# Kernel optimization log

Measured on AMD Instinct MI355X. Metric: run time of the kernel, lower is better.

Reference implementation:

```python
import jax, jax.numpy as jnp
import numpy as np

B, D = 4, 4            # batch, days
N = 5000               # node_number
V = 256                # congestion_space_dimension
F = 64                 # in_channels
C = 32                 # out_channels per head
H = 4                  # heads
E = 80000              # edges per graph (before self loops)
NEG_SLOPE = 0.2        # PyG GATConv default negative_slope


def setup_inputs() -> dict:
    key = jax.random.key(0)
    ks = jax.random.split(key, 7)
    x = jax.random.randint(ks[0], (B, D, N), 0, V)
    adjacency = jax.random.randint(ks[1], (2, E), 0, N)
    emb = jax.random.normal(ks[2], (V, F), dtype=jnp.float32)
    W = jax.random.normal(ks[3], (F, H * C), dtype=jnp.float32) * 0.1
    att_src = jax.random.normal(ks[4], (H, C), dtype=jnp.float32) * 0.1
    att_dst = jax.random.normal(ks[5], (H, C), dtype=jnp.float32) * 0.1
    bias = jnp.zeros((H * C,), dtype=jnp.float32)
    return {"x": x, "adjacency": adjacency, "emb": emb, "W": W,
            "att_src": att_src, "att_dst": att_dst, "bias": bias}


def reference(x, adjacency, emb, W, att_src, att_dst, bias):
    G = B * D
    feats = emb[x].reshape(G, N, F)                       # [G,N,F] embedding lookup
    # PyG GATConv adds self loops by default
    loops = jnp.arange(N)
    src = jnp.concatenate([adjacency[0], loops])          # [Et]
    dst = jnp.concatenate([adjacency[1], loops])          # [Et]
    xw = jnp.einsum('gnf,fk->gnk', feats, W).reshape(G, N, H, C)
    a_s = jnp.einsum('gnhc,hc->gnh', xw, att_src)         # [G,N,H]
    a_d = jnp.einsum('gnhc,hc->gnh', xw, att_dst)
    e = jax.nn.leaky_relu(a_s[:, src] + a_d[:, dst], NEG_SLOPE)  # [G,Et,H]
    # per-destination segment softmax (stable)
    seg_max = jax.vmap(lambda v: jax.ops.segment_max(v, dst, num_segments=N))(e)
    alpha = jnp.exp(e - seg_max[:, dst])
    denom = jax.vmap(lambda v: jax.ops.segment_sum(v, dst, num_segments=N))(alpha)
    alpha = alpha / denom[:, dst]                         # [G,Et,H]
    msg = alpha[..., None] * xw[:, src]                   # [G,Et,H,C]
    out = jax.vmap(lambda m: jax.ops.segment_sum(m, dst, num_segments=N))(msg)
    out = out.reshape(G, N, H * C) + bias                 # concat heads + bias
    return out.reshape(B, D, N * H * C)
```

## Files before the change

kernel.cpp:

```cpp
#include <hip/hip_runtime.h>
#include <math.h>

#define NN 5000
#define GG 16
#define VV 256
#define FF 64
#define HH 4
#define CC 32
#define HC 128
#define EE 80000
#define NEG 0.2f
#define WPB 4
#define SLOT 48
#define SPAD 50

__global__ void k_tables(const float* __restrict__ emb, const float* __restrict__ W,
                         const float* __restrict__ att_src, const float* __restrict__ att_dst,
                         float* __restrict__ T, float* __restrict__ as_t, float* __restrict__ ad_t,
                         int* __restrict__ cnt) {
  if (blockIdx.x >= VV) {
    int n = (blockIdx.x - VV) * 128 + threadIdx.x;
    if (n < NN) cnt[n] = 1;
    return;
  }
  __shared__ float se[FF];
  __shared__ float sT[HC];
  const int v = blockIdx.x;
  const int k = threadIdx.x;
  if (k < FF) se[k] = emb[v * FF + k];
  __syncthreads();
  float acc = 0.f;
#pragma unroll
  for (int f = 0; f < FF; ++f) acc += se[f] * W[f * HC + k];
  T[v * HC + k] = acc;
  sT[k] = acc;
  __syncthreads();
  if (k < 2 * HH) {
    const int h = k >> 1;
    const float* att = (k & 1) ? att_dst : att_src;
    float s = 0.f;
#pragma unroll
    for (int c = 0; c < CC; ++c) s += sT[h * CC + c] * att[h * CC + c];
    if (k & 1) ad_t[v * HH + h] = s;
    else       as_t[v * HH + h] = s;
  }
}

__global__ void k_count(const int* __restrict__ dst, int* __restrict__ cnt) {
  int e = blockIdx.x * blockDim.x + threadIdx.x;
  if (e < EE) atomicAdd(&cnt[dst[e]], 1);
}

__global__ void k_scan(const int* __restrict__ cnt, int* __restrict__ off,
                       int* __restrict__ cursor, int* __restrict__ csr) {
  __shared__ int part[256];
  const int t = threadIdx.x;
  const int CH = (NN + 255) / 256;
  const int i0 = t * CH;
  int lc[CH];
  int lsum = 0;
#pragma unroll
  for (int j = 0; j < CH; ++j) {
    int idx = i0 + j;
    int c = (idx < NN) ? cnt[idx] : 0;
    lc[j] = c;
    lsum += c;
  }
  part[t] = lsum;
  __syncthreads();
  for (int d = 1; d < 256; d <<= 1) {
    int val = (t >= d) ? part[t - d] : 0;
    __syncthreads();
    part[t] += val;
    __syncthreads();
  }
  int run = (t > 0) ? part[t - 1] : 0;
#pragma unroll
  for (int j = 0; j < CH; ++j) {
    int idx = i0 + j;
    if (idx < NN) {
      off[idx] = run;
      cursor[idx] = run + 1;
      csr[run] = idx;
      run += lc[j];
    }
  }
  if (t == 255) off[NN] = part[255];
}

#define NSCAT ((EE + 255) / 256)
__global__ void k_scatter_p(const int* __restrict__ src, const int* __restrict__ dst,
                            int* __restrict__ cursor, int* __restrict__ csr,
                            const float* __restrict__ as_t, const float* __restrict__ ad_t,
                            float* __restrict__ P) {
  if (blockIdx.x < NSCAT) {
    int e = blockIdx.x * 256 + threadIdx.x;
    if (e < EE) {
      int d = dst[e];
      int pos = atomicAdd(&cursor[d], 1);
      csr[pos] = src[e];
    }
    return;
  }
  const int d = blockIdx.x - NSCAT;
  const int v = threadIdx.x;
  const float4 a = ((const float4*)as_t)[v];
  const float4 b = ((const float4*)ad_t)[d];
  float e0 = a.x + b.x; e0 = e0 > 0.f ? e0 : NEG * e0;
  float e1 = a.y + b.y; e1 = e1 > 0.f ? e1 : NEG * e1;
  float e2 = a.z + b.z; e2 = e2 > 0.f ? e2 : NEG * e2;
  float e3 = a.w + b.w; e3 = e3 > 0.f ? e3 : NEG * e3;
  float4 p;
  p.x = __expf(e0); p.y = __expf(e1); p.z = __expf(e2); p.w = __expf(e3);
  ((float4*)P)[d * VV + v] = p;
}

__global__ __launch_bounds__(256)
void k_gat(const int* __restrict__ x, const int* __restrict__ off,
           const int* __restrict__ csr, const float* __restrict__ T,
           const float* __restrict__ P, const float* __restrict__ bias,
           float* __restrict__ out) {
  __shared__ float4 s_p4[WPB][4][SPAD];
  __shared__ int    s_ofs[WPB][4][SPAD];

  const int tid  = threadIdx.x;
  const int wave = tid >> 6;
  const int lane = tid & 63;
  const int sub  = lane >> 4;
  const int sl   = lane & 15;
  const int head = sl >> 2;

  const int w    = blockIdx.x * WPB + wave;
  const int inst = w * 4 + sub;
  const int g    = inst / NN;
  const int n    = inst - g * NN;

  const int base = off[n];
  const int deg  = off[n + 1] - base;
  const int xd   = x[inst];
  const float4* __restrict__ Pd = ((const float4*)P) + xd * VV;
  const int* __restrict__ xg = x + g * NN;

  const int my_ch = sl * 8;
  const float4 b0 = ((const float4*)bias)[sl * 2];
  const float4 b1 = ((const float4*)bias)[sl * 2 + 1];

  float4 dsum = make_float4(0.f, 0.f, 0.f, 0.f);
  float4 a0 = make_float4(0.f, 0.f, 0.f, 0.f);
  float4 a1 = make_float4(0.f, 0.f, 0.f, 0.f);

  for (int c0 = 0; c0 < deg; c0 += SLOT) {
    const int len = min(SLOT, deg - c0);
    for (int r = sl; r < len; r += 16) {
      const int srcn = csr[base + c0 + r];
      const int xv   = xg[srcn];
      const float4 p4 = Pd[xv];
      dsum.x += p4.x; dsum.y += p4.y; dsum.z += p4.z; dsum.w += p4.w;
      s_p4[wave][sub][r]  = p4;
      s_ofs[wave][sub][r] = xv << 7;
    }
    __threadfence_block();
#pragma unroll 2
    for (int j = 0; j < len; ++j) {
      const int   ofs = s_ofs[wave][sub][j];
      const float p   = ((const float*)&s_p4[wave][sub][j])[head];
      const float4 t0 = *(const float4*)&T[ofs + my_ch];
      const float4 t1 = *(const float4*)&T[ofs + my_ch + 4];
      a0.x += p * t0.x; a0.y += p * t0.y; a0.z += p * t0.z; a0.w += p * t0.w;
      a1.x += p * t1.x; a1.y += p * t1.y; a1.z += p * t1.z; a1.w += p * t1.w;
    }
    __threadfence_block();
  }

#pragma unroll
  for (int d = 1; d < 16; d <<= 1) {
    dsum.x += __shfl_xor(dsum.x, d);
    dsum.y += __shfl_xor(dsum.y, d);
    dsum.z += __shfl_xor(dsum.z, d);
    dsum.w += __shfl_xor(dsum.w, d);
  }
  const float den = (head == 0) ? dsum.x : (head == 1) ? dsum.y
                   : (head == 2) ? dsum.z : dsum.w;
  const float r = 1.f / den;

  float4 o0, o1;
  o0.x = a0.x * r + b0.x; o0.y = a0.y * r + b0.y;
  o0.z = a0.z * r + b0.z; o0.w = a0.w * r + b0.w;
  o1.x = a1.x * r + b1.x; o1.y = a1.y * r + b1.y;
  o1.z = a1.z * r + b1.z; o1.w = a1.w * r + b1.w;
  float* op = out + (size_t)inst * HC + my_ch;
  *(float4*)op = o0;
  *(float4*)(op + 4) = o1;
}

extern "C" void kernel_launch(void* const* d_in, const int* in_sizes, int n_in,
                              void* d_out, int out_size, void* d_ws, size_t ws_size,
                              hipStream_t stream) {
  const int*   x       = (const int*)d_in[0];
  const int*   adj     = (const int*)d_in[1];
  const float* emb     = (const float*)d_in[2];
  const float* W       = (const float*)d_in[3];
  const float* att_src = (const float*)d_in[4];
  const float* att_dst = (const float*)d_in[5];
  const float* bias    = (const float*)d_in[6];
  float*       out     = (float*)d_out;

  const int* adj_src = adj;
  const int* adj_dst = adj + EE;

  char* wp = (char*)d_ws;
  float* T    = (float*)wp; wp += (size_t)VV * HC * 4;
  float* as_t = (float*)wp; wp += (size_t)VV * HH * 4;
  float* ad_t = (float*)wp; wp += (size_t)VV * HH * 4;
  int* cnt    = (int*)wp;   wp += (size_t)NN * 4;
  int* off    = (int*)wp;   wp += (size_t)(NN + 4) * 4;
  int* cursor = (int*)wp;   wp += (size_t)NN * 4;
  int* csr    = (int*)wp;   wp += (size_t)(EE + NN) * 4;
  float* P    = (float*)wp; wp += (size_t)VV * VV * HH * 4;

  const int initblk = (NN + 127) / 128;
  k_tables<<<VV + initblk, 128, 0, stream>>>(emb, W, att_src, att_dst, T, as_t, ad_t, cnt);
  k_count<<<(EE + 255) / 256, 256, 0, stream>>>(adj_dst, cnt);
  k_scan<<<1, 256, 0, stream>>>(cnt, off, cursor, csr);
  k_scatter_p<<<NSCAT + VV, 256, 0, stream>>>(adj_src, adj_dst, cursor, csr, as_t, ad_t, P);
  k_gat<<<(GG * NN / 4) / WPB, 256, 0, stream>>>(x, off, csr, T, P, bias, out);
}
```

Before: 139.2 us.

## Fuse preprocessing into cooperative kernel and pre-gather source embedding ids per graph

Merges the four preprocessing launches into one cooperative kernel with grid-wide syncs, and falls back to separate launches if the cooperative launch fails. The CSR scatter now writes, for each of the 16 graphs, the source node's embedding index directly (csr_x). This removes the dependent csr→x double indirection in the main GAT loop and replaces it with one contiguous load. In exchange the scatter writes a 16x larger array (about 5.4 MB), and grid.sync adds its own overhead.

```diff
diff --git a/kernel.cpp b/kernel.cpp
--- a/kernel.cpp
+++ b/kernel.cpp
@@ -1,5 +1,8 @@
 #include <hip/hip_runtime.h>
+#include <hip/hip_cooperative_groups.h>
 #include <math.h>
+
+namespace cg = cooperative_groups;
 
 #define NN 5000
 #define GG 16
@@ -9,55 +12,73 @@
 #define CC 32
 #define HC 128
 #define EE 80000
+#define ET (EE + NN)
 #define NEG 0.2f
 #define WPB 4
 #define SLOT 48
 #define SPAD 50
-
-__global__ void k_tables(const float* __restrict__ emb, const float* __restrict__ W,
-                         const float* __restrict__ att_src, const float* __restrict__ att_dst,
-                         float* __restrict__ T, float* __restrict__ as_t, float* __restrict__ ad_t,
-                         int* __restrict__ cnt) {
-  if (blockIdx.x >= VV) {
-    int n = (blockIdx.x - VV) * 128 + threadIdx.x;
-    if (n < NN) cnt[n] = 1;
-    return;
-  }
-  __shared__ float se[FF];
-  __shared__ float sT[HC];
-  const int v = blockIdx.x;
-  const int k = threadIdx.x;
-  if (k < FF) se[k] = emb[v * FF + k];
-  __syncthreads();
-  float acc = 0.f;
-#pragma unroll
-  for (int f = 0; f < FF; ++f) acc += se[f] * W[f * HC + k];
-  T[v * HC + k] = acc;
-  sT[k] = acc;
-  __syncthreads();
-  if (k < 2 * HH) {
-    const int h = k >> 1;
-    const float* att = (k & 1) ? att_dst : att_src;
-    float s = 0.f;
-#pragma unroll
-    for (int c = 0; c < CC; ++c) s += sT[h * CC + c] * att[h * CC + c];
-    if (k & 1) ad_t[v * HH + h] = s;
-    else       as_t[v * HH + h] = s;
-  }
-}
-
-__global__ void k_count(const int* __restrict__ dst, int* __restrict__ cnt) {
-  int e = blockIdx.x * blockDim.x + threadIdx.x;
-  if (e < EE) atomicAdd(&cnt[dst[e]], 1);
-}
-
-__global__ void k_scan(const int* __restrict__ cnt, int* __restrict__ off,
-                       int* __restrict__ cursor, int* __restrict__ csr) {
-  __shared__ int part[256];
-  const int t = threadIdx.x;
+#define NTASK (GG * NN / 4)
+#define PREP_BLOCKS 512
+
+union PrepS {
+  struct { float se[FF]; float sT[HC]; } tab;
+  int part[256];
+};
+
+__device__ __forceinline__ void phase0(PrepS& sm, int b, int t, int stride,
+                                       const float* __restrict__ emb, const float* __restrict__ W,
+                                       const float* __restrict__ att_src, const float* __restrict__ att_dst,
+                                       float* __restrict__ T, float* __restrict__ as_t,
+                                       float* __restrict__ ad_t, int* __restrict__ cnt) {
+  for (int i = b * 256 + t; i < NN; i += stride) cnt[i] = 0;
+  if (b < VV) {
+    const int v = b;
+    if (t < FF) sm.tab.se[t] = emb[v * FF + t];
+    __syncthreads();
+    if (t < HC) {
+      float acc = 0.f;
+#pragma unroll
+      for (int f = 0; f < FF; ++f) acc += sm.tab.se[f] * W[f * HC + t];
+      T[v * HC + t] = acc;
+      sm.tab.sT[t] = acc;
+    }
+    __syncthreads();
+    if (t < 2 * HH) {
+      const int h = t >> 1;
+      const float* att = (t & 1) ? att_dst : att_src;
+      float s = 0.f;
+#pragma unroll
+      for (int c = 0; c < CC; ++c) s += sm.tab.sT[h * CC + c] * att[h * CC + c];
+      if (t & 1) ad_t[v * HH + h] = s;
+      else       as_t[v * HH + h] = s;
+    }
+  }
+}
+
+__device__ __forceinline__ void phase1(int b, int t, int stride,
+                                       const int* __restrict__ adj_dst, int* __restrict__ cnt,
+                                       const float* __restrict__ as_t, const float* __restrict__ ad_t,
+                                       float* __restrict__ P) {
+  for (int e = b * 256 + t; e < EE; e += stride) atomicAdd(&cnt[adj_dst[e]], 1);
+  if (b >= VV && b < 2 * VV) {
+    const int d = b - VV;
+    const float4 a4 = ((const float4*)as_t)[t];
+    const float4 d4 = ((const float4*)ad_t)[d];
+    float e0 = a4.x + d4.x; e0 = e0 > 0.f ? e0 : NEG * e0;
+    float e1 = a4.y + d4.y; e1 = e1 > 0.f ? e1 : NEG * e1;
+    float e2 = a4.z + d4.z; e2 = e2 > 0.f ? e2 : NEG * e2;
+    float e3 = a4.w + d4.w; e3 = e3 > 0.f ? e3 : NEG * e3;
+    float4 p;
+    p.x = __expf(e0); p.y = __expf(e1); p.z = __expf(e2); p.w = __expf(e3);
+    ((float4*)P)[d * VV + t] = p;
+  }
+}
+
+__device__ __forceinline__ void phase2(PrepS& sm, int t, const int* __restrict__ cnt,
+                                       int* __restrict__ off, int* __restrict__ cursor) {
   const int CH = (NN + 255) / 256;
   const int i0 = t * CH;
-  int lc[CH];
+  int lc[(NN + 255) / 256];
   int lsum = 0;
 #pragma unroll
   for (int j = 0; j < CH; ++j) {
@@ -66,58 +87,93 @@
     lc[j] = c;
     lsum += c;
   }
-  part[t] = lsum;
+  sm.part[t] = lsum;
   __syncthreads();
   for (int d = 1; d < 256; d <<= 1) {
-    int val = (t >= d) ? part[t - d] : 0;
-    __syncthreads();
-    part[t] += val;
-    __syncthreads();
-  }
-  int run = (t > 0) ? part[t - 1] : 0;
+    int val = (t >= d) ? sm.part[t - d] : 0;
+    __syncthreads();
+    sm.part[t] += val;
+    __syncthreads();
+  }
+  int run = (t > 0) ? sm.part[t - 1] : 0;
 #pragma unroll
   for (int j = 0; j < CH; ++j) {
     int idx = i0 + j;
     if (idx < NN) {
-      off[idx] = run;
-      cursor[idx] = run + 1;
-      csr[run] = idx;
+      int o = run + idx;
+      off[idx] = o;
+      cursor[idx] = o + 1;
       run += lc[j];
     }
   }
-  if (t == 255) off[NN] = part[255];
-}
-
-#define NSCAT ((EE + 255) / 256)
-__global__ void k_scatter_p(const int* __restrict__ src, const int* __restrict__ dst,
-                            int* __restrict__ cursor, int* __restrict__ csr,
-                            const float* __restrict__ as_t, const float* __restrict__ ad_t,
-                            float* __restrict__ P) {
-  if (blockIdx.x < NSCAT) {
-    int e = blockIdx.x * 256 + threadIdx.x;
-    if (e < EE) {
-      int d = dst[e];
-      int pos = atomicAdd(&cursor[d], 1);
-      csr[pos] = src[e];
-    }
-    return;
-  }
-  const int d = blockIdx.x - NSCAT;
-  const int v = threadIdx.x;
-  const float4 a = ((const float4*)as_t)[v];
-  const float4 b = ((const float4*)ad_t)[d];
-  float e0 = a.x + b.x; e0 = e0 > 0.f ? e0 : NEG * e0;
-  float e1 = a.y + b.y; e1 = e1 > 0.f ? e1 : NEG * e1;
-  float e2 = a.z + b.z; e2 = e2 > 0.f ? e2 : NEG * e2;
-  float e3 = a.w + b.w; e3 = e3 > 0.f ? e3 : NEG * e3;
-  float4 p;
-  p.x = __expf(e0); p.y = __expf(e1); p.z = __expf(e2); p.w = __expf(e3);
-  ((float4*)P)[d * VV + v] = p;
+  if (t == 255) off[NN] = sm.part[255] + NN;
+}
+
+__device__ __forceinline__ void phase3(int b, int t, int stride,
+                                       const int* __restrict__ x,
+                                       const int* __restrict__ adj_src, const int* __restrict__ adj_dst,
+                                       int* __restrict__ cursor, const int* __restrict__ off,
+                                       int* __restrict__ csr_x) {
+  const int gt = b * 256 + t;
+  for (int e = gt; e < EE; e += stride) {
+    const int d = adj_dst[e], s = adj_src[e];
+    const int pos = atomicAdd(&cursor[d], 1);
+#pragma unroll
+    for (int g = 0; g < GG; ++g) csr_x[g * ET + pos] = x[g * NN + s];
+  }
+  for (int i = gt; i < NN; i += stride) {
+    const int pos = off[i];
+#pragma unroll
+    for (int g = 0; g < GG; ++g) csr_x[g * ET + pos] = x[g * NN + i];
+  }
+}
+
+__global__ __launch_bounds__(256, 2)
+void k_prep(const int* __restrict__ x, const int* __restrict__ adj,
+            const float* __restrict__ emb, const float* __restrict__ W,
+            const float* __restrict__ att_src, const float* __restrict__ att_dst,
+            float* __restrict__ T, float* __restrict__ as_t, float* __restrict__ ad_t,
+            int* __restrict__ cnt, int* __restrict__ off, int* __restrict__ cursor,
+            int* __restrict__ csr_x, float* __restrict__ P) {
+  cg::grid_group grid = cg::this_grid();
+  __shared__ PrepS sm;
+  const int b = blockIdx.x, t = threadIdx.x;
+  const int stride = gridDim.x * 256;
+  const int* adj_src = adj;
+  const int* adj_dst = adj + EE;
+
+  phase0(sm, b, t, stride, emb, W, att_src, att_dst, T, as_t, ad_t, cnt);
+  grid.sync();
+  phase1(b, t, stride, adj_dst, cnt, as_t, ad_t, P);
+  grid.sync();
+  if (b == 0) phase2(sm, t, cnt, off, cursor);
+  grid.sync();
+  phase3(b, t, stride, x, adj_src, adj_dst, cursor, off, csr_x);
+}
+
+__global__ void k_p0(const float* __restrict__ emb, const float* __restrict__ W,
+                     const float* __restrict__ att_src, const float* __restrict__ att_dst,
+                     float* T, float* as_t, float* ad_t, int* cnt) {
+  __shared__ PrepS sm;
+  phase0(sm, blockIdx.x, threadIdx.x, gridDim.x * 256, emb, W, att_src, att_dst, T, as_t, ad_t, cnt);
+}
+__global__ void k_p1(const int* __restrict__ adj_dst, int* cnt,
+                     const float* __restrict__ as_t, const float* __restrict__ ad_t, float* P) {
+  phase1(blockIdx.x, threadIdx.x, gridDim.x * 256, adj_dst, cnt, as_t, ad_t, P);
+}
+__global__ void k_p2(const int* __restrict__ cnt, int* off, int* cursor) {
+  __shared__ PrepS sm;
+  phase2(sm, threadIdx.x, cnt, off, cursor);
+}
+__global__ void k_p3(const int* __restrict__ x, const int* __restrict__ adj_src,
+                     const int* __restrict__ adj_dst, int* cursor, const int* __restrict__ off,
+                     int* csr_x) {
+  phase3(blockIdx.x, threadIdx.x, gridDim.x * 256, x, adj_src, adj_dst, cursor, off, csr_x);
 }
 
 __global__ __launch_bounds__(256)
 void k_gat(const int* __restrict__ x, const int* __restrict__ off,
-           const int* __restrict__ csr, const float* __restrict__ T,
+           const int* __restrict__ csr_x, const float* __restrict__ T,
            const float* __restrict__ P, const float* __restrict__ bias,
            float* __restrict__ out) {
   __shared__ float4 s_p4[WPB][4][SPAD];
@@ -139,7 +195,7 @@
   const int deg  = off[n + 1] - base;
   const int xd   = x[inst];
   const float4* __restrict__ Pd = ((const float4*)P) + xd * VV;
-  const int* __restrict__ xg = x + g * NN;
+  const int* __restrict__ cx = csr_x + g * ET + base;
 
   const int my_ch = sl * 8;
   const float4 b0 = ((const float4*)bias)[sl * 2];
@@ -152,8 +208,7 @@
   for (int c0 = 0; c0 < deg; c0 += SLOT) {
     const int len = min(SLOT, deg - c0);
     for (int r = sl; r < len; r += 16) {
-      const int srcn = csr[base + c0 + r];
-      const int xv   = xg[srcn];
+      const int xv = cx[c0 + r];
       const float4 p4 = Pd[xv];
       dsum.x += p4.x; dsum.y += p4.y; dsum.z += p4.z; dsum.w += p4.w;
       s_p4[wave][sub][r]  = p4;
@@ -205,9 +260,6 @@
   const float* bias    = (const float*)d_in[6];
   float*       out     = (float*)d_out;
 
-  const int* adj_src = adj;
-  const int* adj_dst = adj + EE;
-
   char* wp = (char*)d_ws;
   float* T    = (float*)wp; wp += (size_t)VV * HC * 4;
   float* as_t = (float*)wp; wp += (size_t)VV * HH * 4;
@@ -215,13 +267,24 @@
   int* cnt    = (int*)wp;   wp += (size_t)NN * 4;
   int* off    = (int*)wp;   wp += (size_t)(NN + 4) * 4;
   int* cursor = (int*)wp;   wp += (size_t)NN * 4;
-  int* csr    = (int*)wp;   wp += (size_t)(EE + NN) * 4;
   float* P    = (float*)wp; wp += (size_t)VV * VV * HH * 4;
-
-  const int initblk = (NN + 127) / 128;
-  k_tables<<<VV + initblk, 128, 0, stream>>>(emb, W, att_src, att_dst, T, as_t, ad_t, cnt);
-  k_count<<<(EE + 255) / 256, 256, 0, stream>>>(adj_dst, cnt);
-  k_scan<<<1, 256, 0, stream>>>(cnt, off, cursor, csr);
-  k_scatter_p<<<NSCAT + VV, 256, 0, stream>>>(adj_src, adj_dst, cursor, csr, as_t, ad_t, P);
-  k_gat<<<(GG * NN / 4) / WPB, 256, 0, stream>>>(x, off, csr, T, P, bias, out);
-}
+  int* csr_x  = (int*)wp;   wp += (size_t)GG * ET * 4;
+
+  const int* adj_dst = adj + EE;
+
+  void* args[] = {(void*)&x, (void*)&adj, (void*)&emb, (void*)&W,
+                  (void*)&att_src, (void*)&att_dst,
+                  (void*)&T, (void*)&as_t, (void*)&ad_t,
+                  (void*)&cnt, (void*)&off, (void*)&cursor,
+                  (void*)&csr_x, (void*)&P};
+  hipError_t err = hipLaunchCooperativeKernel((const void*)k_prep, dim3(PREP_BLOCKS), dim3(256),
+                                              args, 0, stream);
+  if (err != hipSuccess) {
+    (void)hipGetLastError();
+    k_p0<<<PREP_BLOCKS, 256, 0, stream>>>(emb, W, att_src, att_dst, T, as_t, ad_t, cnt);
+    k_p1<<<PREP_BLOCKS, 256, 0, stream>>>(adj_dst, cnt, as_t, ad_t, P);
+    k_p2<<<1, 256, 0, stream>>>(cnt, off, cursor);
+    k_p3<<<PREP_BLOCKS, 256, 0, stream>>>(x, adj, adj_dst, cursor, off, csr_x);
+  }
+  k_gat<<<NTASK / WPB, 256, 0, stream>>>(x, off, csr_x, T, P, bias, out);
+}
```

Result: slower. 310.2 us (+122.9%).
